# Optimization experiments

Hardware: AMD Instinct MI355X
Metric: run time of the kernel (lower is better)

The kernel has to match this reference:

```python
import math
import jax, jax.numpy as jnp
import numpy as np

B, E, C = 512, 512, 70722
M_MARGIN, H, S, T_ALPHA, EPS = 0.4, 0.333, 64.0, 1.0, 1e-3


def setup_inputs() -> dict:
    key = jax.random.key(0)
    k0, k1, k2, k3 = jax.random.split(key, 4)
    emb = jax.random.normal(k0, (B, E), dtype=jnp.float32)
    emb = emb / jnp.linalg.norm(emb, axis=1, keepdims=True)  # unit embeddings, as upstream of an arcface head
    kernel = jax.random.normal(k1, (E, 2, C), dtype=jnp.float32)
    # feature norms ~ [5, 35), realistic face-feature magnitudes
    norms = jax.random.uniform(k2, (B, 1), dtype=jnp.float32) * 30.0 + 5.0
    label = jax.random.randint(k3, (B,), 0, C, dtype=jnp.int32)
    return {"embeddings": emb, "norms": norms, "label": label, "kernel": kernel}


def reference(embeddings, norms, label, kernel):
    # column-wise l2 norm of kernel (axis=0 of (E,2,C))
    kn = kernel / jnp.linalg.norm(kernel, axis=0, keepdims=True)
    cosine = jnp.einsum('be,etc->btc', embeddings, kn)
    cosine = jnp.clip(cosine, -1.0 + EPS, 1.0 - EPS)  # (B,2,C)

    safe_norms = jax.lax.stop_gradient(jnp.clip(norms, 1e-3, 100.0))  # (B,1), detached
    sn = safe_norms[:, 0]

    # buffer updates (no_grad block), t_alpha-EMA; initial values batch_mean=20, std=10, classwise=20
    counts = jax.ops.segment_sum(jnp.ones_like(sn), label, num_segments=C)
    sums = jax.ops.segment_sum(sn, label, num_segments=C)
    batch_group_mean = sums / jnp.maximum(counts, 1.0)  # row-l1-normalized M @ norms
    present = counts > 0
    classwise_mean = jnp.where(present, batch_group_mean * T_ALPHA + (1.0 - T_ALPHA) * 20.0, 20.0)
    batch_mean = jnp.mean(sn) * T_ALPHA + (1.0 - T_ALPHA) * 20.0
    batch_std = jnp.std(sn, ddof=1) * T_ALPHA + (1.0 - T_ALPHA) * 10.0

    margin_scaler = jnp.clip((safe_norms - batch_mean) / (batch_std + EPS) * H, -1.0, 1.0)  # (B,1)
    cw_margin_scaler = jnp.clip((safe_norms - classwise_mean[label][:, None]) / (batch_std + EPS), -1.0, 1.0) * H

    w1 = cosine[:, 0, :]  # (B,C)
    cos2_tgt = cosine[jnp.arange(B), 1, label]  # (B,)
    one_hot = jax.nn.one_hot(label, C, dtype=w1.dtype)  # (B,C)
    mask = one_hot > 0
    # target column taken from the second prototype; grad hook masks non-target grads
    w2 = jnp.where(mask, cos2_tgt[:, None], jax.lax.stop_gradient(w1))

    g_angular = -M_MARGIN * margin_scaler  # (B,1)
    origin_m_arc = one_hot * g_angular  # (B,C)
    g_add = M_MARGIN + M_MARGIN * margin_scaler
    origin_m_cos = one_hot * g_add

    theta_m = jnp.clip(jnp.arccos(w1) + origin_m_arc, EPS, math.pi - EPS)
    scaled_cosine_m = (jnp.cos(theta_m) - origin_m_cos) * S

    theta_m2 = jnp.clip(jnp.arccos(w2) + origin_m_arc, EPS, math.pi - EPS)
    scaled_cosine_m2 = (jnp.cos(theta_m2) - origin_m_cos) * S

    return scaled_cosine_m, scaled_cosine_m2, cw_margin_scaler
```

## Files before the change

kernel.cpp:

```cpp
#include <hip/hip_runtime.h>

#define B_SZ 512
#define E_SZ 512
#define C_SZ 70722
#define NPAD 70784
#define NTILES 553
#define EPSC 0.001f
#define MMARG 0.4f
#define HC 0.333f
#define SC 64.0f
#define PI_F 3.14159265358979323846f

typedef __attribute__((ext_vector_type(8))) short short8;
typedef __attribute__((ext_vector_type(4))) float f32x4;

__device__ __forceinline__ unsigned short f32_to_bf16(float f) {
  unsigned int u = __builtin_bit_cast(unsigned int, f);
  u += 0x7fffu + ((u >> 16) & 1u);
  return (unsigned short)(u >> 16);
}

__device__ __forceinline__ void load16(void* lds, const void* g) {
  __builtin_amdgcn_global_load_lds(
      (const __attribute__((address_space(1))) void*)g,
      (__attribute__((address_space(3))) void*)lds, 16, 0, 0);
}

__global__ __launch_bounds__(512) void k_stats(
    const float* __restrict__ norms, const int* __restrict__ label,
    float* __restrict__ g_ang, float* __restrict__ g_add,
    float* __restrict__ out_cw) {
  __shared__ float sn[512];
  __shared__ int   lab[512];
  __shared__ float red[512];
  const int t = threadIdx.x;
  float x = norms[t];
  x = fminf(fmaxf(x, 0.001f), 100.0f);
  sn[t] = x; lab[t] = label[t]; red[t] = x;
  __syncthreads();
  for (int s = 256; s > 0; s >>= 1) { if (t < s) red[t] += red[t + s]; __syncthreads(); }
  const float mean = red[0] * (1.0f / 512.0f);
  __syncthreads();
  const float d = x - mean;
  red[t] = d * d;
  __syncthreads();
  for (int s = 256; s > 0; s >>= 1) { if (t < s) red[t] += red[t + s]; __syncthreads(); }
  const float stdv = sqrtf(red[0] / 511.0f);
  const float denom = stdv + EPSC;
  float cnt = 0.f, sum = 0.f;
  const int myl = lab[t];
  for (int j = 0; j < 512; ++j) { if (lab[j] == myl) { cnt += 1.0f; sum += sn[j]; } }
  const float cwm = sum / cnt;
  const float ms = fminf(fmaxf((x - mean) / denom * HC, -1.0f), 1.0f);
  out_cw[t] = fminf(fmaxf((x - cwm) / denom, -1.0f), 1.0f) * HC;
  g_ang[t] = -MMARG * ms;
  g_add[t] = MMARG + MMARG * ms;
}

__global__ __launch_bounds__(256) void k_convert_emb(
    const float* __restrict__ emb, unsigned short* __restrict__ Abf) {
  const int i = blockIdx.x * 256 + threadIdx.x;
  Abf[i] = f32_to_bf16(emb[i]);
}

__global__ __launch_bounds__(256) void k_prep_b(
    const float* __restrict__ Kr, unsigned short* __restrict__ Bt,
    float* __restrict__ invn) {
  __shared__ __align__(16) float Tr[64 * 65];
  __shared__ float part[256];
  const int t = threadIdx.x;
  const int c0 = blockIdx.x * 64;
  float accv = 0.f;
  for (int et = 0; et < 8; ++et) {
    const int e0 = et * 64;
#pragma unroll
    for (int i = 0; i < 16; ++i) {
      const int idx = t + i * 256;
      const int r  = idx >> 6;
      const int cc = idx & 63;
      const float v = Kr[(size_t)(e0 + r) * (2 * C_SZ) + (c0 + cc)];
      Tr[cc * 65 + r] = v;
      accv += v * v;
    }
    __syncthreads();
#pragma unroll
    for (int i = 0; i < 16; ++i) {
      const int idx = t + i * 256;
      const int cc = idx >> 6;
      const int ee = idx & 63;
      Bt[(size_t)(c0 + cc) * E_SZ + e0 + ee] = f32_to_bf16(Tr[cc * 65 + ee]);
    }
    __syncthreads();
  }
  part[t] = accv;
  __syncthreads();
  if (t < 64) {
    const float s = part[t] + part[t + 64] + part[t + 128] + part[t + 192];
    invn[c0 + t] = rsqrtf(s);
  }
}

__global__ __launch_bounds__(64) void k_cos2(
    const float* __restrict__ emb, const float* __restrict__ Kr,
    const int* __restrict__ label, float* __restrict__ cos2t) {
  const int b = blockIdx.x;
  const int l = threadIdx.x;
  const int lb = label[b];
  float s1 = 0.f, s2 = 0.f;
#pragma unroll
  for (int e = l; e < E_SZ; e += 64) {
    const float a  = emb[b * E_SZ + e];
    const float kv = Kr[(size_t)e * (2 * C_SZ) + C_SZ + lb];
    s1 += a * kv;
    s2 += kv * kv;
  }
#pragma unroll
  for (int off = 32; off > 0; off >>= 1) {
    s1 += __shfl_down(s1, off);
    s2 += __shfl_down(s2, off);
  }
  if (l == 0) {
    float cv = s1 * rsqrtf(s2);
    cv = fminf(fmaxf(cv, -1.0f + EPSC), 1.0f - EPSC);
    cos2t[b] = cv;
  }
}

__global__ __launch_bounds__(256) void k_gemm(
    const unsigned short* __restrict__ Abf, const unsigned short* __restrict__ Bt,
    const float* __restrict__ invn, const int* __restrict__ label,
    const float* __restrict__ g_ang, const float* __restrict__ g_add,
    const float* __restrict__ cos2t,
    float* __restrict__ out0, float* __restrict__ out1, float* __restrict__ tgtv1) {
  __shared__ __align__(16) unsigned short As[128 * 32];
  __shared__ __align__(16) unsigned short Bs[128 * 32];
  __shared__ int   lab_s[128];
  __shared__ float ga_s[128];
  __shared__ float gd_s[128];
  __shared__ float c2_s[128];
  __shared__ float inv_s[128];

  const int tid = threadIdx.x;
  const int m0 = blockIdx.x * 128;
  const int n0 = blockIdx.y * 128;

  if (tid < 128) {
    lab_s[tid] = label[m0 + tid];
    ga_s[tid]  = g_ang[m0 + tid];
    gd_s[tid]  = g_add[m0 + tid];
    c2_s[tid]  = cos2t[m0 + tid];
    inv_s[tid] = invn[n0 + tid];
  }

  f32x4 acc[4][4];
#pragma unroll
  for (int i = 0; i < 4; ++i)
#pragma unroll
    for (int j = 0; j < 4; ++j) acc[i][j] = (f32x4){0.f, 0.f, 0.f, 0.f};

  const int l  = tid & 63;
  const int w  = tid >> 6;
  const int wm = (w >> 1) * 64;
  const int wn = (w & 1) * 64;

  const int srow = tid >> 2;
  const int scol = (tid & 3) * 8;
  const unsigned short* Ag0 = Abf + (size_t)(m0 + srow) * E_SZ + scol;
  const unsigned short* Bg0 = Bt  + (size_t)(n0 + srow) * E_SZ + scol;

  char* AsB = (char*)As;
  char* BsB = (char*)Bs;
  const int ldsoff = tid * 16;
  const int lr  = l & 15;
  const int lqb = (l >> 4) * 16;

  for (int kt = 0; kt < 16; ++kt) {
    const int k0 = kt * 32;
    load16(AsB + ldsoff,        Ag0 + k0);
    load16(AsB + 4096 + ldsoff, Ag0 + 64 * E_SZ + k0);
    load16(BsB + ldsoff,        Bg0 + k0);
    load16(BsB + 4096 + ldsoff, Bg0 + 64 * E_SZ + k0);
    __syncthreads();

    short8 af[4], bfv[4];
#pragma unroll
    for (int mi = 0; mi < 4; ++mi)
      af[mi] = *(const short8*)(AsB + (wm + mi * 16 + lr) * 64 + lqb);
#pragma unroll
    for (int ni = 0; ni < 4; ++ni)
      bfv[ni] = *(const short8*)(BsB + (wn + ni * 16 + lr) * 64 + lqb);
#pragma unroll
    for (int mi = 0; mi < 4; ++mi)
#pragma unroll
      for (int ni = 0; ni < 4; ++ni)
        acc[mi][ni] = __builtin_amdgcn_mfma_f32_16x16x32_bf16(af[mi], bfv[ni], acc[mi][ni], 0, 0, 0);
    __syncthreads();
  }

  const int lq4 = (l >> 4) * 4;
#pragma unroll
  for (int mi = 0; mi < 4; ++mi) {
    const int blb = wm + mi * 16 + lq4;
#pragma unroll
    for (int ni = 0; ni < 4; ++ni) {
      const int cl = wn + ni * 16 + lr;
      const int c  = n0 + cl;
      if (c < C_SZ) {
        const float inv = inv_s[cl];
        const f32x4 a = acc[mi][ni];
#pragma unroll
        for (int r = 0; r < 4; ++r) {
          const int bl = blb + r;
          const int b  = m0 + bl;
          float w1 = a[r] * inv;
          w1 = fminf(fmaxf(w1, -1.0f + EPSC), 1.0f - EPSC);
          float v0 = w1 * SC;
          float v1 = v0;
          if (c == lab_s[bl]) {
            const float ga = ga_s[bl];
            const float gd = gd_s[bl];
            float th = acosf(w1) + ga;
            th = fminf(fmaxf(th, EPSC), PI_F - EPSC);
            v0 = (cosf(th) - gd) * SC;
            const float w2 = c2_s[bl];
            float th2 = acosf(w2) + ga;
            th2 = fminf(fmaxf(th2, EPSC), PI_F - EPSC);
            v1 = (cosf(th2) - gd) * SC;
            if (tgtv1) tgtv1[b] = v1;
          }
          const size_t off = (size_t)b * C_SZ + c;
          out0[off] = v0;
          if (out1) out1[off] = v1;
        }
      }
    }
  }
}

__global__ __launch_bounds__(256) void k_patch(
    const float* __restrict__ out0, const int* __restrict__ label,
    const float* __restrict__ tgtv1, float* __restrict__ out1) {
  const int b = blockIdx.y;
  const int i2 = (blockIdx.x * 256 + threadIdx.x) * 2;
  if (i2 >= C_SZ) return;
  const size_t off = (size_t)b * C_SZ + i2;
  float2 v = *(const float2*)(out0 + off);
  const int lb = label[b];
  if (lb == i2)          v.x = tgtv1[b];
  else if (lb == i2 + 1) v.y = tgtv1[b];
  *(float2*)(out1 + off) = v;
}

extern "C" void kernel_launch(void* const* d_in, const int* in_sizes, int n_in,
                              void* d_out, int out_size, void* d_ws, size_t ws_size,
                              hipStream_t stream) {
  const float* emb   = (const float*)d_in[0];
  const float* norms = (const float*)d_in[1];
  const int*   label = (const int*)d_in[2];
  const float* Kr    = (const float*)d_in[3];

  float* out  = (float*)d_out;
  float* out0 = out;
  float* out1 = out + (size_t)B_SZ * C_SZ;
  float* outcw = out + (size_t)2 * B_SZ * C_SZ;

  char* ws = (char*)d_ws;
  unsigned short* Abf = (unsigned short*)(ws);
  float* invn  = (float*)(ws + 524288);
  float* g_ang = (float*)(ws + 807424);
  float* g_add = (float*)(ws + 809472);
  float* c2    = (float*)(ws + 811520);
  float* tgtv1 = (float*)(ws + 813568);
  const size_t bt_off = 1048576;
  const size_t need_direct = bt_off + (size_t)NPAD * E_SZ * 2;
  const bool direct = ws_size >= need_direct;
  unsigned short* Bt = direct
      ? (unsigned short*)(ws + bt_off)
      : (unsigned short*)((char*)d_out + (size_t)B_SZ * C_SZ * 4);

  k_stats<<<1, 512, 0, stream>>>(norms, label, g_ang, g_add, outcw);
  k_convert_emb<<<(B_SZ * E_SZ) / 256, 256, 0, stream>>>(emb, Abf);
  k_prep_b<<<NPAD / 64, 256, 0, stream>>>(Kr, Bt, invn);
  k_cos2<<<B_SZ, 64, 0, stream>>>(emb, Kr, label, c2);
  k_gemm<<<dim3(4, NTILES), 256, 0, stream>>>(Abf, Bt, invn, label, g_ang, g_add, c2,
                                              out0, direct ? out1 : (float*)nullptr,
                                              direct ? (float*)nullptr : tgtv1);
  if (!direct) {
    k_patch<<<dim3((C_SZ / 2 + 255) / 256, B_SZ), 256, 0, stream>>>(out0, label, tgtv1, out1);
  }
}
```

Measured before the change: 610.3 us.

## Vectorize prep kernels, double-buffer GEMM LDS, remap tiles per XCD, nontemporal stores

The embedding conversion and kernel transpose/normalization kernels now use 16-byte vector loads and stores, with a new LDS layout and reduction for column norms. The GEMM double-buffers its LDS tiles so the next K-slice is prefetched while MFMAs run on the current one. A 1D grid with an XCD-aware remap groups neighbouring tiles onto the same chiplet, and output writes use nontemporal stores to avoid polluting cache. Together these target memory-bound prep stages and load latency in the GEMM, at the cost of doubled LDS use per block.

```diff
diff --git a/kernel.cpp b/kernel.cpp
--- a/kernel.cpp
+++ b/kernel.cpp
@@ -59,43 +59,62 @@
 
 __global__ __launch_bounds__(256) void k_convert_emb(
     const float* __restrict__ emb, unsigned short* __restrict__ Abf) {
-  const int i = blockIdx.x * 256 + threadIdx.x;
-  Abf[i] = f32_to_bf16(emb[i]);
+  const int i = (blockIdx.x * 256 + threadIdx.x) * 8;
+  const f32x4 a = *(const f32x4*)(emb + i);
+  const f32x4 b = *(const f32x4*)(emb + i + 4);
+  short8 o;
+  o[0] = (short)f32_to_bf16(a[0]); o[1] = (short)f32_to_bf16(a[1]);
+  o[2] = (short)f32_to_bf16(a[2]); o[3] = (short)f32_to_bf16(a[3]);
+  o[4] = (short)f32_to_bf16(b[0]); o[5] = (short)f32_to_bf16(b[1]);
+  o[6] = (short)f32_to_bf16(b[2]); o[7] = (short)f32_to_bf16(b[3]);
+  *(short8*)(Abf + i) = o;
 }
 
 __global__ __launch_bounds__(256) void k_prep_b(
     const float* __restrict__ Kr, unsigned short* __restrict__ Bt,
     float* __restrict__ invn) {
-  __shared__ __align__(16) float Tr[64 * 65];
-  __shared__ float part[256];
-  const int t = threadIdx.x;
+  __shared__ __align__(16) float Tr[64][68];
+  __shared__ float part[64][8];
+  const int t  = threadIdx.x;
   const int c0 = blockIdx.x * 64;
-  float accv = 0.f;
+  const int lr = t >> 4;
+  const int lq = t & 15;
+  const int rc = t & 31;
+  const int ro = t >> 5;
+  float accv[2] = {0.f, 0.f};
+
   for (int et = 0; et < 8; ++et) {
     const int e0 = et * 64;
 #pragma unroll
-    for (int i = 0; i < 16; ++i) {
-      const int idx = t + i * 256;
-      const int r  = idx >> 6;
-      const int cc = idx & 63;
-      const float v = Kr[(size_t)(e0 + r) * (2 * C_SZ) + (c0 + cc)];
-      Tr[cc * 65 + r] = v;
-      accv += v * v;
+    for (int i = 0; i < 4; ++i) {
+      const int rr = lr + 16 * i;
+      const f32x4 v = *(const f32x4*)(Kr + (size_t)(e0 + rr) * (2 * C_SZ) + c0 + lq * 4);
+      *(f32x4*)(&Tr[rr][lq * 4]) = v;
     }
     __syncthreads();
 #pragma unroll
-    for (int i = 0; i < 16; ++i) {
-      const int idx = t + i * 256;
-      const int cc = idx >> 6;
-      const int ee = idx & 63;
-      Bt[(size_t)(c0 + cc) * E_SZ + e0 + ee] = f32_to_bf16(Tr[cc * 65 + ee]);
+    for (int i = 0; i < 2; ++i) {
+      const int c = rc + 32 * i;
+      short8 pk;
+      float sq = 0.f;
+#pragma unroll
+      for (int j = 0; j < 8; ++j) {
+        const float v = Tr[ro * 8 + j][c];
+        sq += v * v;
+        pk[j] = (short)f32_to_bf16(v);
+      }
+      accv[i] += sq;
+      *(short8*)(Bt + (size_t)(c0 + c) * E_SZ + e0 + ro * 8) = pk;
     }
     __syncthreads();
   }
-  part[t] = accv;
+  part[rc][ro]      = accv[0];
+  part[rc + 32][ro] = accv[1];
   __syncthreads();
   if (t < 64) {
-    const float s = part[t] + part[t + 64] + part[t + 128] + part[t + 192];
+    float s = 0.f;
+#pragma unroll
+    for (int o = 0; o < 8; ++o) s += part[t][o];
     invn[c0 + t] = rsqrtf(s);
   }
 }
@@ -132,8 +151,8 @@
     const float* __restrict__ g_ang, const float* __restrict__ g_add,
     const float* __restrict__ cos2t,
     float* __restrict__ out0, float* __restrict__ out1, float* __restrict__ tgtv1) {
-  __shared__ __align__(16) unsigned short As[128 * 32];
-  __shared__ __align__(16) unsigned short Bs[128 * 32];
+  __shared__ __align__(16) unsigned short As[2][4096];
+  __shared__ __align__(16) unsigned short Bs[2][4096];
   __shared__ int   lab_s[128];
   __shared__ float ga_s[128];
   __shared__ float gd_s[128];
@@ -141,8 +160,12 @@
   __shared__ float inv_s[128];
 
   const int tid = threadIdx.x;
-  const int m0 = blockIdx.x * 128;
-  const int n0 = blockIdx.y * 128;
+  const int nwg = 4 * NTILES;
+  const int q = nwg >> 3, r = nwg & 7;
+  const int xcd = blockIdx.x & 7, pos = blockIdx.x >> 3;
+  const int logical = (xcd < r ? xcd * (q + 1) : r * (q + 1) + (xcd - r) * q) + pos;
+  const int m0 = (logical & 3) * 128;
+  const int n0 = (logical >> 2) * 128;
 
   if (tid < 128) {
     lab_s[tid] = label[m0 + tid];
@@ -168,20 +191,31 @@
   const unsigned short* Ag0 = Abf + (size_t)(m0 + srow) * E_SZ + scol;
   const unsigned short* Bg0 = Bt  + (size_t)(n0 + srow) * E_SZ + scol;
 
-  char* AsB = (char*)As;
-  char* BsB = (char*)Bs;
   const int ldsoff = tid * 16;
   const int lr  = l & 15;
   const int lqb = (l >> 4) * 16;
 
+  {
+    char* AsB = (char*)As[0]; char* BsB = (char*)Bs[0];
+    load16(AsB + ldsoff,        Ag0);
+    load16(AsB + 4096 + ldsoff, Ag0 + 64 * E_SZ);
+    load16(BsB + ldsoff,        Bg0);
+    load16(BsB + 4096 + ldsoff, Bg0 + 64 * E_SZ);
+  }
+  __syncthreads();
+
+  int cur = 0;
   for (int kt = 0; kt < 16; ++kt) {
-    const int k0 = kt * 32;
-    load16(AsB + ldsoff,        Ag0 + k0);
-    load16(AsB + 4096 + ldsoff, Ag0 + 64 * E_SZ + k0);
-    load16(BsB + ldsoff,        Bg0 + k0);
-    load16(BsB + 4096 + ldsoff, Bg0 + 64 * E_SZ + k0);
-    __syncthreads();
-
+    if (kt < 15) {
+      const int kn = (kt + 1) * 32;
+      char* AsB = (char*)As[cur ^ 1]; char* BsB = (char*)Bs[cur ^ 1];
+      load16(AsB + ldsoff,        Ag0 + kn);
+      load16(AsB + 4096 + ldsoff, Ag0 + 64 * E_SZ + kn);
+      load16(BsB + ldsoff,        Bg0 + kn);
+      load16(BsB + 4096 + ldsoff, Bg0 + 64 * E_SZ + kn);
+    }
+    const char* AsB = (const char*)As[cur];
+    const char* BsB = (const char*)Bs[cur];
     short8 af[4], bfv[4];
 #pragma unroll
     for (int mi = 0; mi < 4; ++mi)
@@ -195,6 +229,7 @@
       for (int ni = 0; ni < 4; ++ni)
         acc[mi][ni] = __builtin_amdgcn_mfma_f32_16x16x32_bf16(af[mi], bfv[ni], acc[mi][ni], 0, 0, 0);
     __syncthreads();
+    cur ^= 1;
   }
 
   const int lq4 = (l >> 4) * 4;
@@ -209,10 +244,10 @@
         const float inv = inv_s[cl];
         const f32x4 a = acc[mi][ni];
 #pragma unroll
-        for (int r = 0; r < 4; ++r) {
-          const int bl = blb + r;
+        for (int rg = 0; rg < 4; ++rg) {
+          const int bl = blb + rg;
           const int b  = m0 + bl;
-          float w1 = a[r] * inv;
+          float w1 = a[rg] * inv;
           w1 = fminf(fmaxf(w1, -1.0f + EPSC), 1.0f - EPSC);
           float v0 = w1 * SC;
           float v1 = v0;
@@ -229,8 +264,8 @@
             if (tgtv1) tgtv1[b] = v1;
           }
           const size_t off = (size_t)b * C_SZ + c;
-          out0[off] = v0;
-          if (out1) out1[off] = v1;
+          __builtin_nontemporal_store(v0, out0 + off);
+          if (out1) __builtin_nontemporal_store(v1, out1 + off);
         }
       }
     }
@@ -279,12 +314,12 @@
       : (unsigned short*)((char*)d_out + (size_t)B_SZ * C_SZ * 4);
 
   k_stats<<<1, 512, 0, stream>>>(norms, label, g_ang, g_add, outcw);
-  k_convert_emb<<<(B_SZ * E_SZ) / 256, 256, 0, stream>>>(emb, Abf);
+  k_convert_emb<<<(B_SZ * E_SZ) / (256 * 8), 256, 0, stream>>>(emb, Abf);
   k_prep_b<<<NPAD / 64, 256, 0, stream>>>(Kr, Bt, invn);
   k_cos2<<<B_SZ, 64, 0, stream>>>(emb, Kr, label, c2);
-  k_gemm<<<dim3(4, NTILES), 256, 0, stream>>>(Abf, Bt, invn, label, g_ang, g_add, c2,
-                                              out0, direct ? out1 : (float*)nullptr,
-                                              direct ? (float*)nullptr : tgtv1);
+  k_gemm<<<dim3(4 * NTILES), 256, 0, stream>>>(Abf, Bt, invn, label, g_ang, g_add, c2,
+                                               out0, direct ? out1 : (float*)nullptr,
+                                               direct ? (float*)nullptr : tgtv1);
   if (!direct) {
     k_patch<<<dim3((C_SZ / 2 + 255) / 256, B_SZ), 256, 0, stream>>>(out0, label, tgtv1, out1);
   }
```

After: 788.4 us. 1.29x slower.
